# Kernel optimization log

Hardware: AMD Instinct MI355X
Metric: run time of the kernel (lower is better)

Reference implementation:

```python
import jax, jax.numpy as jnp
import numpy as np

K = 8192          # num_embeddings
D = 256           # embedding_dim
DECAY = 0.95
EPS = 1e-05
COMMIT = 0.25


def setup_inputs() -> dict:
    key = jax.random.key(0)
    k1, k2, k3 = jax.random.split(key, 3)
    x = jax.random.normal(k1, (32, D, 32, 32), dtype=jnp.float32)
    codebook = jax.random.uniform(k2, (K, D), dtype=jnp.float32,
                                  minval=-1.0 / K, maxval=1.0 / K)
    ema_count = jnp.zeros((K,), dtype=jnp.float32)
    ema_weight = jax.random.normal(k3, (K, D), dtype=jnp.float32)
    return {"x": x, "codebook": codebook, "ema_count": ema_count,
            "ema_weight": ema_weight}


def reference(x, codebook, ema_count, ema_weight):
    b, c, h, w = x.shape
    inputs = jnp.transpose(x, (0, 2, 3, 1))          # [B,H,W,C]
    flat = inputs.reshape(-1, c)                     # [N,C], N=B*H*W
    n = flat.shape[0]

    # squared euclidean distances: ||z||^2 + ||e||^2 - 2 z.e
    distances = (jnp.sum(flat * flat, axis=1, keepdims=True)
                 + jnp.sum(codebook * codebook, axis=1)
                 - 2.0 * flat @ codebook.T)          # [N,K]
    idx = jnp.argmin(distances, axis=1)              # [N]

    # one-hot @ codebook == gather
    quantized = codebook[idx].reshape(inputs.shape)  # [B,H,W,C]

    # EMA codebook update (training branch, no-grad in torch)
    counts = jax.ops.segment_sum(jnp.ones((n,), flat.dtype), idx,
                                 num_segments=K)     # encodings.sum(0)
    new_count = ema_count * DECAY + (1.0 - DECAY) * counts
    new_count = (new_count + EPS) / (n + K * EPS) * n
    dw = jax.ops.segment_sum(flat, idx, num_segments=K)  # encodings.T @ flat
    new_weight = ema_weight * DECAY + (1.0 - DECAY) * dw
    new_codebook = new_weight / new_count[:, None]

    e_loss = COMMIT * jnp.mean((jax.lax.stop_gradient(quantized) - inputs) ** 2)
    quantized_st = inputs + jax.lax.stop_gradient(quantized - inputs)

    indices = idx.reshape(b, h * w)
    return (e_loss,
            jnp.transpose(quantized_st, (0, 3, 1, 2)),
            indices,
            new_count, new_weight, new_codebook)
```

## Files before the change

### kernel.cpp

```cpp
#include <hip/hip_runtime.h>
#include <stdint.h>

#define N_TOK 32768
#define DIM   256
#define KCB   8192
#define HWSZ  1024

#define WS_FLATB   0u
#define WS_CBB     4194304u
#define WS_A32     5242880u
#define WS_B32     5275648u
#define WS_IDX     5283840u
#define WS_CAND    5316608u
#define WS_ICNT    5840896u
#define WS_CUR     5849088u
#define WS_OFFS    5857280u
#define WS_PERM    5865472u
#define WS_LPART   5898240u
#define WS_DW      5914624u
#define WS_TOTAL   8011776u
#define WS_MEMSET_LEN 16384u

#define O_LOSS 0u
#define O_Q    1u
#define O_IDX  8388609u
#define O_CNT  8421377u
#define O_W    8429569u
#define O_CB   10526721u

typedef __attribute__((ext_vector_type(8))) short bf16x8;
typedef __attribute__((ext_vector_type(4))) float f32x4;

__device__ __forceinline__ void g2lds16(const void* gp, void* lp){
  __builtin_amdgcn_global_load_lds(
      (const __attribute__((address_space(1))) void*)gp,
      (__attribute__((address_space(3))) void*)lp, 16, 0, 0);
}

__device__ __forceinline__ unsigned short f2b(float f){
  unsigned u = __float_as_uint(f);
  return (unsigned short)((u + 0x7FFFu + ((u >> 16) & 1u)) >> 16);
}

__device__ __forceinline__ unsigned umin2(unsigned a, unsigned b){ return a < b ? a : b; }
__device__ __forceinline__ unsigned umax2(unsigned a, unsigned b){ return a > b ? a : b; }

__global__ void k_flatb(const float* __restrict__ x, unsigned short* __restrict__ flatB){
  __shared__ float tile[64][65];
  const int bx = blockIdx.x;
  const int b = bx >> 6, ct = (bx >> 4) & 3, ht = bx & 15;
  const int c0 = ct * 64, hw0 = ht * 64;
  const int t = threadIdx.x, rr = t >> 4, cc4 = (t & 15) * 4;
  #pragma unroll
  for (int j = 0; j < 4; j++){
    const int crow = rr + j * 16;
    float4 v = *(const float4*)(x + ((size_t)(b * 256 + c0 + crow) << 10) + hw0 + cc4);
    tile[crow][cc4] = v.x; tile[crow][cc4+1] = v.y; tile[crow][cc4+2] = v.z; tile[crow][cc4+3] = v.w;
  }
  __syncthreads();
  #pragma unroll
  for (int j = 0; j < 4; j++){
    const int hwrow = rr + j * 16;
    ushort4 o = { f2b(tile[cc4][hwrow]), f2b(tile[cc4+1][hwrow]),
                  f2b(tile[cc4+2][hwrow]), f2b(tile[cc4+3][hwrow]) };
    *(ushort4*)(flatB + ((size_t)(b * 1024 + hw0 + hwrow) << 8) + c0 + cc4) = o;
  }
}

__global__ void k_cbb(const float* __restrict__ cb, unsigned short* __restrict__ cbB){
  const int t = blockIdx.x * 256 + threadIdx.x;
  float4 v = *(const float4*)(cb + (size_t)t * 4);
  ushort4 o = { f2b(v.x), f2b(v.y), f2b(v.z), f2b(v.w) };
  *(ushort4*)(cbB + (size_t)t * 4) = o;
}

__device__ __forceinline__ float np_pairwise_sq(const float* __restrict__ p, int stride){
  #pragma clang fp contract(off)
  float h[2];
  #pragma unroll
  for (int half = 0; half < 2; half++){
    const float* q = p + half * 128 * stride;
    float r[8];
    #pragma unroll
    for (int j = 0; j < 8; j++){ float z = q[j * stride]; r[j] = z * z; }
    for (int i = 8; i < 128; i += 8){
      #pragma unroll
      for (int j = 0; j < 8; j++){ float z = q[(i + j) * stride]; r[j] = r[j] + z * z; }
    }
    h[half] = ((r[0] + r[1]) + (r[2] + r[3])) + ((r[4] + r[5]) + (r[6] + r[7]));
  }
  return h[0] + h[1];
}

__global__ void k_sqn(const float* __restrict__ x, const float* __restrict__ cb,
                      float* __restrict__ a32, float* __restrict__ b32){
  int t = blockIdx.x * 256 + threadIdx.x;
  if (t < N_TOK){
    int b = t >> 10, hw = t & 1023;
    a32[t] = np_pairwise_sq(x + (size_t)b * 262144 + hw, 1024);
  } else {
    int k2 = t - N_TOK;
    b32[k2] = np_pairwise_sq(cb + (size_t)k2 * 256, 1);
  }
}

__launch_bounds__(256, 2)
__global__ void k_dist(const unsigned short* __restrict__ flatB,
                       const unsigned short* __restrict__ cbB,
                       const float* __restrict__ b32,
                       int* __restrict__ cand)
{
  __shared__ __align__(16) unsigned short A1[128 * 128];
  __shared__ __align__(16) unsigned short Bs[2][128 * 64];

  const int tid = threadIdx.x;
  const int bx = blockIdx.x;
  const int tt = bx >> 1, h = bx & 1;
  const int tok0 = tt * 128;
  const int wv = tid >> 6, lane = tid & 63;
  const int wy = wv >> 1, wx = wv & 1;
  const int l4 = lane >> 4, lm = lane & 15;

  const unsigned short* fB = flatB + (size_t)tok0 * 256;
  const unsigned short* cB = cbB + (size_t)h * 4096 * 256;

  {
    const int r = lane >> 4, p = lane & 15;
    #pragma unroll
    for (int j = 0; j < 8; j++){
      const int row = wv * 32 + j * 4 + r;
      const int gc = p ^ (row & 15);
      g2lds16((const char*)fB + (size_t)row * 512 + (gc << 4),
              (char*)A1 + (wv * 32 + j * 4) * 256);
    }
    unsigned short* A2 = &Bs[0][0];
    #pragma unroll
    for (int j = 0; j < 8; j++){
      const int row = wv * 32 + j * 4 + r;
      const int gc = p ^ (row & 15);
      g2lds16((const char*)fB + (size_t)row * 512 + 256 + (gc << 4),
              (char*)A2 + (wv * 32 + j * 4) * 256);
    }
  }
  __syncthreads();

  bf16x8 a2[4][4];
  {
    const unsigned short* A2 = &Bs[0][0];
    #pragma unroll
    for (int ks4 = 0; ks4 < 4; ks4++)
      #pragma unroll
      for (int ii = 0; ii < 4; ii++){
        const int m = wy * 64 + ii * 16 + lm;
        const int c = ks4 * 4 + l4;
        a2[ks4][ii] = *(const bf16x8*)((const char*)A2 + m * 256 + ((c ^ (m & 15)) << 4));
      }
  }
  __syncthreads();

  unsigned aoff[4][4];
  #pragma unroll
  for (int kg = 0; kg < 4; kg++)
    #pragma unroll
    for (int ii = 0; ii < 4; ii++){
      const int m = wy * 64 + ii * 16 + lm;
      const int ca = kg * 4 + l4;
      aoff[kg][ii] = (unsigned)(m * 256 + ((ca ^ (m & 15)) << 4));
    }
  unsigned boff[2][2][4];
  #pragma unroll
  for (int buf = 0; buf < 2; buf++)
    #pragma unroll
    for (int ks2 = 0; ks2 < 2; ks2++)
      #pragma unroll
      for (int jj = 0; jj < 4; jj++){
        const int n = wx * 64 + jj * 16 + lm;
        const int c2 = ks2 * 4 + l4;
        boff[buf][ks2][jj] = (unsigned)(buf * 16384 + n * 128 + ((c2 ^ (n & 7)) << 4));
      }
  const char* gBj[4];
  unsigned dstj[4];
  {
    const int r8 = lane >> 3, p = lane & 7;
    #pragma unroll
    for (int j = 0; j < 4; j++){
      const int row = wv * 32 + j * 8 + r8;
      const int gc = p ^ (row & 7);
      gBj[j] = (const char*)cB + (size_t)row * 512 + (gc << 4);
      dstj[j] = (unsigned)((wv * 32 + j * 8) * 128);
    }
  }

  auto stageB = [&](int S2){
    const int ss = S2 & 3, cc = S2 >> 2;
    const int buf = (S2 & 1) * 16384;
    const size_t soff = (size_t)(cc * 65536 + ss * 128);
    #pragma unroll
    for (int j = 0; j < 4; j++)
      g2lds16(gBj[j] + soff, (char*)Bs + buf + dstj[j]);
  };

  unsigned k1[16], k2[16];
  #pragma unroll
  for (int i = 0; i < 16; i++){ k1[i] = 0xFFFFFFFFu; k2[i] = 0xFFFFFFFFu; }

  f32x4 acc[4][4];
  float bn125[4];

  stageB(0);
  __syncthreads();

  for (int c = 0; c < 32; c++){
    #pragma unroll
    for (int s = 0; s < 4; s++){
      const int S = c * 4 + s;
      if (S + 1 < 128) stageB(S + 1);
      if (s == 0){
        #pragma unroll
        for (int jj = 0; jj < 4; jj++)
          bn125[jj] = b32[h * 4096 + c * 128 + wx * 64 + jj * 16 + lm] + 0.125f;
        #pragma unroll
        for (int ii = 0; ii < 4; ii++)
          #pragma unroll
          for (int jj = 0; jj < 4; jj++)
            acc[ii][jj] = (f32x4){0.f, 0.f, 0.f, 0.f};
      }
      #pragma unroll
      for (int ks2 = 0; ks2 < 2; ks2++){
        const int kg = s * 2 + ks2;
        bf16x8 bf[4], af[4];
        #pragma unroll
        for (int jj = 0; jj < 4; jj++)
          bf[jj] = *(const bf16x8*)((const char*)Bs + boff[s & 1][ks2][jj]);
        if (kg < 4){
          #pragma unroll
          for (int ii = 0; ii < 4; ii++)
            af[ii] = *(const bf16x8*)((const char*)A1 + aoff[kg][ii]);
        } else {
          #pragma unroll
          for (int ii = 0; ii < 4; ii++) af[ii] = a2[kg - 4][ii];
        }
        #pragma unroll
        for (int ii = 0; ii < 4; ii++)
          #pragma unroll
          for (int jj = 0; jj < 4; jj++)
            acc[ii][jj] = __builtin_amdgcn_mfma_f32_16x16x32_bf16(af[ii], bf[jj], acc[ii][jj], 0, 0, 0);
      }
      if (s == 3){
        unsigned pk[4];
        #pragma unroll
        for (int jj = 0; jj < 4; jj++) pk[jj] = (unsigned)((c << 2) | jj);
        #pragma unroll
        for (int ii = 0; ii < 4; ii++){
          #pragma unroll
          for (int r = 0; r < 4; r++){
            const int rk = ii * 4 + r;
            unsigned kb[4];
            #pragma unroll
            for (int jj = 0; jj < 4; jj++){
              const float v = fmaf(-2.f, acc[ii][jj][r], bn125[jj]);
              kb[jj] = (__float_as_uint(v) & 0xFFFFFF80u) | pk[jj];
            }
            const unsigned lo01 = umin2(kb[0], kb[1]), hi01 = umax2(kb[0], kb[1]);
            const unsigned lo23 = umin2(kb[2], kb[3]), hi23 = umax2(kb[2], kb[3]);
            const unsigned s1 = umin2(lo01, lo23);
            const unsigned s2 = umin2(umax2(lo01, lo23), umin2(hi01, hi23));
            const unsigned t = umax2(k1[rk], s1);
            k1[rk] = umin2(k1[rk], s1);
            k2[rk] = umin2(umin2(k2[rk], t), s2);
          }
        }
      }
      __syncthreads();
    }
  }

  const unsigned colbase = (unsigned)(wx * 64 + lm);
  auto fin = [colbase](unsigned key)->unsigned {
    const float v125 = __uint_as_float(key & 0xFFFFFF80u);
    int qi = (int)(v125 * 4194304.f);
    qi = qi < 0 ? 0 : (qi > 0xFFFFF ? 0xFFFFF : qi);
    const unsigned cc = (key >> 2) & 31u, jj = key & 3u;
    return ((unsigned)qi << 12) | (cc * 128u + jj * 16u + colbase);
  };
  unsigned* red = (unsigned*)&A1[0];
  #pragma unroll
  for (int rk = 0; rk < 16; rk++){
    const int srow = wy * 64 + (rk >> 2) * 16 + l4 * 4 + (rk & 3);
    red[srow * 64 + wx * 32 + lm * 2 + 0] = fin(k1[rk]);
    red[srow * 64 + wx * 32 + lm * 2 + 1] = fin(k2[rk]);
  }
  __syncthreads();
  if (tid < 128){
    unsigned best[8];
    #pragma unroll
    for (int j = 0; j < 8; j++) best[j] = 0xFFFFFFFFu;
    for (int i = 0; i < 64; i++){
      unsigned k = red[tid * 64 + i];
      if (k < best[7]){
        best[7] = k;
        #pragma unroll
        for (int j = 7; j > 0; j--){
          if (best[j] < best[j-1]){ unsigned tmp = best[j]; best[j] = best[j-1]; best[j-1] = tmp; }
        }
      }
    }
    const size_t base = ((size_t)(tok0 + tid) * 2 + h) * 8;
    #pragma unroll
    for (int j = 0; j < 8; j++) cand[base + j] = h * 4096 + (int)(best[j] & 0xFFFu);
  }
}

__global__ void k_pick(const float* __restrict__ x, const float* __restrict__ cb,
                       const float* __restrict__ a32, const float* __restrict__ b32,
                       const int* __restrict__ cand, int* __restrict__ idx,
                       int* __restrict__ icnt, float* __restrict__ out_idx)
{
  const int gt = blockIdx.x * 256 + threadIdx.x;
  const int n = gt >> 6;
  const int lane = gt & 63;
  const int b = n >> 10, hw = n & 1023;
  const int c0 = lane * 4;
  float z0 = x[(((size_t)b * DIM + c0 + 0) << 10) + hw];
  float z1 = x[(((size_t)b * DIM + c0 + 1) << 10) + hw];
  float z2 = x[(((size_t)b * DIM + c0 + 2) << 10) + hw];
  float z3 = x[(((size_t)b * DIM + c0 + 3) << 10) + hw];
  const float an = a32[n];
  float bestd = 3.4e38f; int besti = 0x7fffffff;
  for (int j = 0; j < 16; j++){
    const int ci = cand[(size_t)n * 16 + j];
    if (ci < 0 || ci >= KCB) continue;
    float4 e = *(const float4*)(cb + (size_t)ci * DIM + c0);
    double se = (double)z0*e.x + (double)z1*e.y + (double)z2*e.z + (double)z3*e.w;
    #pragma unroll
    for (int o = 32; o > 0; o >>= 1) se += __shfl_xor(se, o, 64);
    const float A = an + b32[ci];
    const float d32 = (float)((double)A - 2.0 * se);
    if (d32 < bestd || (d32 == bestd && ci < besti)){ bestd = d32; besti = ci; }
  }
  if (lane == 0){
    idx[n] = besti;
    atomicAdd(icnt + besti, 1);
    out_idx[n] = (float)besti;
  }
}

__global__ void k_scan(const int* __restrict__ icnt, int* __restrict__ offs){
  __shared__ int sums[256];
  const int tid = threadIdx.x;
  int loc[32];
  int s = 0;
  #pragma unroll
  for (int i = 0; i < 32; i++){ loc[i] = s; s += icnt[tid * 32 + i]; }
  sums[tid] = s;
  #pragma unroll
  for (int off = 1; off < 256; off <<= 1){
    __syncthreads();
    const int add = (tid >= off) ? sums[tid - off] : 0;
    __syncthreads();
    sums[tid] += add;
  }
  __syncthreads();
  const int pre = (tid == 0) ? 0 : sums[tid - 1];
  #pragma unroll
  for (int i = 0; i < 32; i++) offs[tid * 32 + i] = pre + loc[i];
}

__global__ void k_perm(const int* __restrict__ idx, const int* __restrict__ offs,
                       int* __restrict__ cur, int* __restrict__ perm){
  int t = blockIdx.x * 256 + threadIdx.x;
  int code = idx[t];
  int slot = atomicAdd(cur + code, 1);
  perm[offs[code] + slot] = t;
}

__global__ void k_dw(const unsigned short* __restrict__ flatB,
                     const int* __restrict__ offs, const int* __restrict__ icnt,
                     const int* __restrict__ perm, float* __restrict__ dw)
{
  const int k = blockIdx.x;
  const int c = threadIdx.x;
  const int start = offs[k], cnt = icnt[k];
  float s = 0.f;
  for (int i = 0; i < cnt; i++){
    const int n = perm[start + i];
    s += __uint_as_float(((unsigned)flatB[((size_t)n << 8) + c]) << 16);
  }
  dw[((size_t)k << 8) + c] = s;
}

__global__ void k_quant(const float* __restrict__ x, const float* __restrict__ cb,
                        const int* __restrict__ idx, float* __restrict__ outq,
                        double* __restrict__ lpart)
{
  __shared__ double wred[4];
  int t = blockIdx.x * 256 + threadIdx.x;
  int c = t >> 13;
  int g = t & 8191; int n = g * 4;
  int b = n >> 10, hw = n & 1023;
  size_t xo = (((size_t)b * DIM + c) << 10) + hw;
  float4 xv = *(const float4*)(x + xo);
  int i0 = idx[n], i1 = idx[n+1], i2 = idx[n+2], i3 = idx[n+3];
  float q0 = cb[(size_t)i0 * DIM + c];
  float q1 = cb[(size_t)i1 * DIM + c];
  float q2 = cb[(size_t)i2 * DIM + c];
  float q3 = cb[(size_t)i3 * DIM + c];
  float qd0 = q0 - xv.x, qd1 = q1 - xv.y, qd2 = q2 - xv.z, qd3 = q3 - xv.w;
  float4 ov = { xv.x + qd0, xv.y + qd1, xv.z + qd2, xv.w + qd3 };
  *(float4*)(outq + xo) = ov;
  double p = (double)(qd0*qd0 + qd1*qd1 + qd2*qd2 + qd3*qd3);
  #pragma unroll
  for (int o = 32; o > 0; o >>= 1) p += __shfl_down(p, o, 64);
  if ((threadIdx.x & 63) == 0) wred[threadIdx.x >> 6] = p;
  __syncthreads();
  if (threadIdx.x == 0) lpart[blockIdx.x] = (wred[0] + wred[1]) + (wred[2] + wred[3]);
}

__global__ void k_count(const int* __restrict__ icnt, const float* __restrict__ ema_count,
                        const double* __restrict__ lpart, float* __restrict__ out)
{
  int k = blockIdx.x * 256 + threadIdx.x;
  float t1 = ema_count[k] * 0.95f;
  float t2 = 0.05f * (float)icnt[k];
  float s  = t1 + t2;
  float s2 = s + 1e-5f;
  const float DEN = (float)(32768.0 + 8192.0 * 1e-5);
  float nc = (s2 / DEN) * 32768.0f;
  out[O_CNT + k] = nc;
  if (blockIdx.x == 0){
    __shared__ double sred[256];
    const int tid = threadIdx.x;
    double ls = 0.0;
    for (int i = tid; i < 8192; i += 256) ls += lpart[i];
    sred[tid] = ls;
    __syncthreads();
    for (int off = 128; off > 0; off >>= 1){
      if (tid < off) sred[tid] += sred[tid + off];
      __syncthreads();
    }
    if (tid == 0) out[O_LOSS] = 0.25f * (float)(sred[0] / 8388608.0);
  }
}

__global__ void k_final(const float* __restrict__ ema_w, const float* __restrict__ dw,
                        const float* __restrict__ out_cnt,
                        float* __restrict__ out_w, float* __restrict__ out_cb)
{
  #pragma clang fp contract(off)
  int t = blockIdx.x * 256 + threadIdx.x;
  int k = t >> 8;
  float w = ema_w[t];
  float d = dw[t];
  float t1 = w * 0.95f;
  float t2 = 0.05f * d;
  float nw = t1 + t2;
  out_w[t]  = nw;
  out_cb[t] = nw / out_cnt[k];
}

extern "C" void kernel_launch(void* const* d_in, const int* in_sizes, int n_in,
                              void* d_out, int out_size, void* d_ws, size_t ws_size,
                              hipStream_t stream)
{
  const float* x         = (const float*)d_in[0];
  const float* cb        = (const float*)d_in[1];
  const float* ema_count = (const float*)d_in[2];
  const float* ema_w     = (const float*)d_in[3];
  float* out = (float*)d_out;
  float* ws  = (float*)d_ws;

  unsigned short* flatB = (unsigned short*)(ws + WS_FLATB);
  unsigned short* cbB   = (unsigned short*)(ws + WS_CBB);
  float*  a32    = ws + WS_A32;
  float*  b32    = ws + WS_B32;
  int*    idxp   = (int*)(ws + WS_IDX);
  int*    candp  = (int*)(ws + WS_CAND);
  int*    icnt   = (int*)(ws + WS_ICNT);
  int*    curp   = (int*)(ws + WS_CUR);
  int*    offs   = (int*)(ws + WS_OFFS);
  int*    permp  = (int*)(ws + WS_PERM);
  double* lpart  = (double*)(ws + WS_LPART);
  float*  dwp    = ws + WS_DW;

  (void)hipMemsetAsync(ws + WS_ICNT, 0, (size_t)WS_MEMSET_LEN * sizeof(float), stream);

  k_flatb<<<2048, 256, 0, stream>>>(x, flatB);
  k_cbb  <<<2048, 256, 0, stream>>>(cb, cbB);
  k_sqn  <<<160,  256, 0, stream>>>(x, cb, a32, b32);
  k_dist <<<512,  256, 0, stream>>>(flatB, cbB, b32, candp);
  k_pick <<<8192, 256, 0, stream>>>(x, cb, a32, b32, candp, idxp, icnt, out + O_IDX);
  k_scan <<<1,    256, 0, stream>>>(icnt, offs);
  k_perm <<<128,  256, 0, stream>>>(idxp, offs, curp, permp);
  k_dw   <<<8192, 256, 0, stream>>>(flatB, offs, icnt, permp, dwp);
  k_quant<<<8192, 256, 0, stream>>>(x, cb, idxp, out + O_Q, lpart);
  k_count<<<32,   256, 0, stream>>>(icnt, ema_count, lpart, out);
  k_final<<<8192, 256, 0, stream>>>(ema_w, dwp, out + O_CNT, out + O_W, out + O_CB);
}
```

Before: 450.4 us.

## Merge prep kernels, tile quantize gather through LDS, fuse count into final

Combines the bf16 conversion and squared-norm kernels into one launch with block-range dispatch. Rewrites the quantize kernel so each block gathers 64 codebook rows into shared memory with coalesced reads, then writes the NCHW output coalesced. Merges the count and final-update kernels, which removes a launch and the re-read of new counts. The aim is fewer launches and fewer strided gathers, at the cost of an extra barrier and slightly more shared memory per quantize block.

```diff
diff --git a/kernel.cpp b/kernel.cpp
--- a/kernel.cpp
+++ b/kernel.cpp
@@ -45,35 +45,6 @@
 __device__ __forceinline__ unsigned umin2(unsigned a, unsigned b){ return a < b ? a : b; }
 __device__ __forceinline__ unsigned umax2(unsigned a, unsigned b){ return a > b ? a : b; }
 
-__global__ void k_flatb(const float* __restrict__ x, unsigned short* __restrict__ flatB){
-  __shared__ float tile[64][65];
-  const int bx = blockIdx.x;
-  const int b = bx >> 6, ct = (bx >> 4) & 3, ht = bx & 15;
-  const int c0 = ct * 64, hw0 = ht * 64;
-  const int t = threadIdx.x, rr = t >> 4, cc4 = (t & 15) * 4;
-  #pragma unroll
-  for (int j = 0; j < 4; j++){
-    const int crow = rr + j * 16;
-    float4 v = *(const float4*)(x + ((size_t)(b * 256 + c0 + crow) << 10) + hw0 + cc4);
-    tile[crow][cc4] = v.x; tile[crow][cc4+1] = v.y; tile[crow][cc4+2] = v.z; tile[crow][cc4+3] = v.w;
-  }
-  __syncthreads();
-  #pragma unroll
-  for (int j = 0; j < 4; j++){
-    const int hwrow = rr + j * 16;
-    ushort4 o = { f2b(tile[cc4][hwrow]), f2b(tile[cc4+1][hwrow]),
-                  f2b(tile[cc4+2][hwrow]), f2b(tile[cc4+3][hwrow]) };
-    *(ushort4*)(flatB + ((size_t)(b * 1024 + hw0 + hwrow) << 8) + c0 + cc4) = o;
-  }
-}
-
-__global__ void k_cbb(const float* __restrict__ cb, unsigned short* __restrict__ cbB){
-  const int t = blockIdx.x * 256 + threadIdx.x;
-  float4 v = *(const float4*)(cb + (size_t)t * 4);
-  ushort4 o = { f2b(v.x), f2b(v.y), f2b(v.z), f2b(v.w) };
-  *(ushort4*)(cbB + (size_t)t * 4) = o;
-}
-
 __device__ __forceinline__ float np_pairwise_sq(const float* __restrict__ p, int stride){
   #pragma clang fp contract(off)
   float h[2];
@@ -92,15 +63,45 @@
   return h[0] + h[1];
 }
 
-__global__ void k_sqn(const float* __restrict__ x, const float* __restrict__ cb,
-                      float* __restrict__ a32, float* __restrict__ b32){
-  int t = blockIdx.x * 256 + threadIdx.x;
-  if (t < N_TOK){
-    int b = t >> 10, hw = t & 1023;
-    a32[t] = np_pairwise_sq(x + (size_t)b * 262144 + hw, 1024);
+__global__ void k_prep(const float* __restrict__ x, const float* __restrict__ cb,
+                       unsigned short* __restrict__ flatB, unsigned short* __restrict__ cbB,
+                       float* __restrict__ a32, float* __restrict__ b32)
+{
+  __shared__ float tile[64][65];
+  const int bx = blockIdx.x;
+  const int t = threadIdx.x;
+  if (bx < 2048){
+    const int b = bx >> 6, ct = (bx >> 4) & 3, ht = bx & 15;
+    const int c0 = ct * 64, hw0 = ht * 64;
+    const int rr = t >> 4, cc4 = (t & 15) * 4;
+    #pragma unroll
+    for (int j = 0; j < 4; j++){
+      const int crow = rr + j * 16;
+      float4 v = *(const float4*)(x + ((size_t)(b * 256 + c0 + crow) << 10) + hw0 + cc4);
+      tile[crow][cc4] = v.x; tile[crow][cc4+1] = v.y; tile[crow][cc4+2] = v.z; tile[crow][cc4+3] = v.w;
+    }
+    __syncthreads();
+    #pragma unroll
+    for (int j = 0; j < 4; j++){
+      const int hwrow = rr + j * 16;
+      ushort4 o = { f2b(tile[cc4][hwrow]), f2b(tile[cc4+1][hwrow]),
+                    f2b(tile[cc4+2][hwrow]), f2b(tile[cc4+3][hwrow]) };
+      *(ushort4*)(flatB + ((size_t)(b * 1024 + hw0 + hwrow) << 8) + c0 + cc4) = o;
+    }
+  } else if (bx < 4096){
+    const int g = (bx - 2048) * 256 + t;
+    float4 v = *(const float4*)(cb + (size_t)g * 4);
+    ushort4 o = { f2b(v.x), f2b(v.y), f2b(v.z), f2b(v.w) };
+    *(ushort4*)(cbB + (size_t)g * 4) = o;
   } else {
-    int k2 = t - N_TOK;
-    b32[k2] = np_pairwise_sq(cb + (size_t)k2 * 256, 1);
+    const int g = (bx - 4096) * 256 + t;
+    if (g < N_TOK){
+      int b = g >> 10, hw = g & 1023;
+      a32[g] = np_pairwise_sq(x + (size_t)b * 262144 + hw, 1024);
+    } else {
+      int k2 = g - N_TOK;
+      b32[k2] = np_pairwise_sq(cb + (size_t)k2 * 256, 1);
+    }
   }
 }
 
@@ -393,45 +394,76 @@
                         const int* __restrict__ idx, float* __restrict__ outq,
                         double* __restrict__ lpart)
 {
+  __shared__ float qt[64][65];
   __shared__ double wred[4];
-  int t = blockIdx.x * 256 + threadIdx.x;
-  int c = t >> 13;
-  int g = t & 8191; int n = g * 4;
-  int b = n >> 10, hw = n & 1023;
-  size_t xo = (((size_t)b * DIM + c) << 10) + hw;
-  float4 xv = *(const float4*)(x + xo);
-  int i0 = idx[n], i1 = idx[n+1], i2 = idx[n+2], i3 = idx[n+3];
-  float q0 = cb[(size_t)i0 * DIM + c];
-  float q1 = cb[(size_t)i1 * DIM + c];
-  float q2 = cb[(size_t)i2 * DIM + c];
-  float q3 = cb[(size_t)i3 * DIM + c];
-  float qd0 = q0 - xv.x, qd1 = q1 - xv.y, qd2 = q2 - xv.z, qd3 = q3 - xv.w;
-  float4 ov = { xv.x + qd0, xv.y + qd1, xv.z + qd2, xv.w + qd3 };
-  *(float4*)(outq + xo) = ov;
-  double p = (double)(qd0*qd0 + qd1*qd1 + qd2*qd2 + qd3*qd3);
+  const int bx = blockIdx.x;
+  const int tid = threadIdx.x;
+  const int b = bx >> 6, ct = (bx >> 4) & 3, ht = bx & 15;
+  const int c0 = ct * 64, hw0 = ht * 64;
+  const int n0 = b * 1024 + hw0;
+
+  {
+    const int cl = tid & 63, wq = tid >> 6;
+    for (int r16 = 0; r16 < 16; r16++){
+      const int row = r16 * 4 + wq;
+      const int i = idx[n0 + row];
+      qt[row][cl] = cb[(size_t)i * DIM + c0 + cl];
+    }
+  }
+  __syncthreads();
+
+  const int cc = tid >> 4;
+  const int hw4 = (tid & 15) * 4;
+  double p = 0.0;
+  #pragma unroll
+  for (int j = 0; j < 4; j++){
+    const int cl = cc + j * 16;
+    const size_t xo = (((size_t)(b * 256 + c0 + cl)) << 10) + hw0 + hw4;
+    float4 xv = *(const float4*)(x + xo);
+    float q0 = qt[hw4 + 0][cl];
+    float q1 = qt[hw4 + 1][cl];
+    float q2 = qt[hw4 + 2][cl];
+    float q3 = qt[hw4 + 3][cl];
+    float qd0 = q0 - xv.x, qd1 = q1 - xv.y, qd2 = q2 - xv.z, qd3 = q3 - xv.w;
+    float4 ov = { xv.x + qd0, xv.y + qd1, xv.z + qd2, xv.w + qd3 };
+    *(float4*)(outq + xo) = ov;
+    p += (double)(qd0*qd0 + qd1*qd1 + qd2*qd2 + qd3*qd3);
+  }
   #pragma unroll
   for (int o = 32; o > 0; o >>= 1) p += __shfl_down(p, o, 64);
-  if ((threadIdx.x & 63) == 0) wred[threadIdx.x >> 6] = p;
-  __syncthreads();
-  if (threadIdx.x == 0) lpart[blockIdx.x] = (wred[0] + wred[1]) + (wred[2] + wred[3]);
-}
-
-__global__ void k_count(const int* __restrict__ icnt, const float* __restrict__ ema_count,
+  if ((tid & 63) == 0) wred[tid >> 6] = p;
+  __syncthreads();
+  if (tid == 0) lpart[bx] = (wred[0] + wred[1]) + (wred[2] + wred[3]);
+}
+
+__global__ void k_final(const float* __restrict__ ema_w, const float* __restrict__ dw,
+                        const int* __restrict__ icnt, const float* __restrict__ ema_count,
                         const double* __restrict__ lpart, float* __restrict__ out)
 {
-  int k = blockIdx.x * 256 + threadIdx.x;
-  float t1 = ema_count[k] * 0.95f;
-  float t2 = 0.05f * (float)icnt[k];
-  float s  = t1 + t2;
+  const int k = blockIdx.x;
+  const int tid = threadIdx.x;
+  float ct1 = ema_count[k] * 0.95f;
+  float ct2 = 0.05f * (float)icnt[k];
+  float s  = ct1 + ct2;
   float s2 = s + 1e-5f;
   const float DEN = (float)(32768.0 + 8192.0 * 1e-5);
   float nc = (s2 / DEN) * 32768.0f;
-  out[O_CNT + k] = nc;
-  if (blockIdx.x == 0){
+  if (tid == 0) out[O_CNT + k] = nc;
+  {
+    #pragma clang fp contract(off)
+    const int t = k * 256 + tid;
+    float w = ema_w[t];
+    float d = dw[t];
+    float t1 = w * 0.95f;
+    float t2 = 0.05f * d;
+    float nw = t1 + t2;
+    out[O_W + t]  = nw;
+    out[O_CB + t] = nw / nc;
+  }
+  if (k == 0){
     __shared__ double sred[256];
-    const int tid = threadIdx.x;
     double ls = 0.0;
-    for (int i = tid; i < 8192; i += 256) ls += lpart[i];
+    for (int i = tid; i < 2048; i += 256) ls += lpart[i];
     sred[tid] = ls;
     __syncthreads();
     for (int off = 128; off > 0; off >>= 1){
@@ -440,22 +472,6 @@
     }
     if (tid == 0) out[O_LOSS] = 0.25f * (float)(sred[0] / 8388608.0);
   }
-}
-
-__global__ void k_final(const float* __restrict__ ema_w, const float* __restrict__ dw,
-                        const float* __restrict__ out_cnt,
-                        float* __restrict__ out_w, float* __restrict__ out_cb)
-{
-  #pragma clang fp contract(off)
-  int t = blockIdx.x * 256 + threadIdx.x;
-  int k = t >> 8;
-  float w = ema_w[t];
-  float d = dw[t];
-  float t1 = w * 0.95f;
-  float t2 = 0.05f * d;
-  float nw = t1 + t2;
-  out_w[t]  = nw;
-  out_cb[t] = nw / out_cnt[k];
 }
 
 extern "C" void kernel_launch(void* const* d_in, const int* in_sizes, int n_in,
@@ -484,15 +500,12 @@
 
   (void)hipMemsetAsync(ws + WS_ICNT, 0, (size_t)WS_MEMSET_LEN * sizeof(float), stream);
 
-  k_flatb<<<2048, 256, 0, stream>>>(x, flatB);
-  k_cbb  <<<2048, 256, 0, stream>>>(cb, cbB);
-  k_sqn  <<<160,  256, 0, stream>>>(x, cb, a32, b32);
+  k_prep <<<4256, 256, 0, stream>>>(x, cb, flatB, cbB, a32, b32);
   k_dist <<<512,  256, 0, stream>>>(flatB, cbB, b32, candp);
   k_pick <<<8192, 256, 0, stream>>>(x, cb, a32, b32, candp, idxp, icnt, out + O_IDX);
   k_scan <<<1,    256, 0, stream>>>(icnt, offs);
   k_perm <<<128,  256, 0, stream>>>(idxp, offs, curp, permp);
   k_dw   <<<8192, 256, 0, stream>>>(flatB, offs, icnt, permp, dwp);
-  k_quant<<<8192, 256, 0, stream>>>(x, cb, idxp, out + O_Q, lpart);
-  k_count<<<32,   256, 0, stream>>>(icnt, ema_count, lpart, out);
-  k_final<<<8192, 256, 0, stream>>>(ema_w, dwp, out + O_CNT, out + O_W, out + O_CB);
-}
+  k_quant<<<2048, 256, 0, stream>>>(x, cb, idxp, out + O_Q, lpart);
+  k_final<<<8192, 256, 0, stream>>>(ema_w, dwp, icnt, ema_count, lpart, out);
+}
```

Result: faster. 411.4 us (-8.7%).
